# Performance work log

Measured on AMD Instinct MI355X. Metric: run time of the kernel, lower is better.

The kernel has to match this reference:

```python
import jax, jax.numpy as jnp
import numpy as np

B, S, D, H = 2, 2048, 1024, 16
HD = D // H  # head_dim = 64


def setup_inputs() -> dict:
    key = jax.random.key(0)
    k1, k2, k3 = jax.random.split(key, 3)
    x = jax.random.normal(k1, (B, S, D), dtype=jnp.float32)
    W_qkv = jax.random.normal(k2, (D, 3 * D), dtype=jnp.float32) * (D ** -0.5)
    b_qkv = jnp.zeros((3 * D,), dtype=jnp.float32)
    W_proj = jax.random.normal(k3, (D, D), dtype=jnp.float32) * (D ** -0.5)
    b_proj = jnp.zeros((D,), dtype=jnp.float32)
    return {"x": x, "W_qkv": W_qkv, "b_qkv": b_qkv, "W_proj": W_proj, "b_proj": b_proj}


def reference(x, W_qkv, b_qkv, W_proj, b_proj):
    b, s, d = x.shape
    scale = HD ** -0.5
    qkv = x @ W_qkv + b_qkv                       # [B,S,3D]
    q, k, v = jnp.split(qkv, 3, axis=-1)
    # [B,S,D] -> [B,H,S,HD]
    def to_heads(t):
        return t.reshape(b, s, H, HD).transpose(0, 2, 1, 3)
    q, k, v = map(to_heads, (q, k, v))
    scores = jnp.einsum('bhqd,bhkd->bhqk', q, k) * scale  # [B,H,S,S]
    causal = jnp.triu(jnp.ones((s, s), dtype=bool), k=1)
    scores = jnp.where(causal[None, None], -jnp.inf, scores)
    attn = jax.nn.softmax(scores, axis=-1)
    out = jnp.einsum('bhqk,bhkd->bhqd', attn, v)  # [B,H,S,HD]
    out = out.transpose(0, 2, 1, 3).reshape(b, s, d)
    return out @ W_proj + b_proj
```

## Files before the change

kernel.cpp:

```cpp
#include <hip/hip_runtime.h>

using frag_t = __attribute__((ext_vector_type(8))) short;
using f32x4  = __attribute__((ext_vector_type(4))) float;

#define L2E 1.4426950408889634f

#if __has_builtin(__builtin_amdgcn_exp2f)
#define EXP2(x) __builtin_amdgcn_exp2f(x)
#else
#define EXP2(x) exp2f(x)
#endif

constexpr int B_  = 2, S_ = 2048, D_ = 1024, H_ = 16, HD_ = 64;
constexpr float QSCALE = 0.125f * L2E;

__device__ __forceinline__ ushort f2bf(float f) {
  union { float f; unsigned u; } v; v.f = f;
  unsigned u = v.u;
  unsigned r = (u + 0x7FFFu + ((u >> 16) & 1u)) >> 16;
  return (ushort)r;
}

__device__ __forceinline__ void gld_lds16(const ushort* g, ushort* l) {
  __builtin_amdgcn_global_load_lds((const __attribute__((address_space(1))) void*)g,
                                   (__attribute__((address_space(3))) void*)l, 16, 0, 0);
}

__global__ __launch_bounds__(256) void k_prep(
    const float* __restrict__ x, const float* __restrict__ Wqkv,
    const float* __restrict__ Wproj,
    ushort* __restrict__ Xbf, ushort* __restrict__ Wqt, ushort* __restrict__ Wpt) {
  int blk = blockIdx.x, tid = threadIdx.x;
  if (blk < 1024) {
    size_t base = (size_t)blk * 4096 + tid * 4;
    #pragma unroll
    for (int i = 0; i < 4; ++i) {
      float4 f = *(const float4*)(x + base + i * 1024);
      ushort4 o;
      o.x = f2bf(f.x); o.y = f2bf(f.y); o.z = f2bf(f.z); o.w = f2bf(f.w);
      *(ushort4*)(Xbf + base + i * 1024) = o;
    }
  } else {
    __shared__ float tile[64][65];
    const float* in; ushort* out; int N, K, bx, by;
    if (blk < 1024 + 768) { int b2 = blk - 1024; in = Wqkv;  out = Wqt; N = 3072; K = 1024; bx = b2 % 48; by = b2 / 48; }
    else                  { int b2 = blk - 1792; in = Wproj; out = Wpt; N = 1024; K = 1024; bx = b2 % 16; by = b2 / 16; }
    int n0 = bx * 64, k0 = by * 64;
    int tx = tid & 63, ty = tid >> 6;
    #pragma unroll
    for (int i = 0; i < 16; ++i)
      tile[ty + i * 4][tx] = in[(size_t)(k0 + ty + i * 4) * N + n0 + tx];
    __syncthreads();
    #pragma unroll
    for (int i = 0; i < 16; ++i)
      out[(size_t)(n0 + ty + i * 4) * K + k0 + tx] = f2bf(tile[tx][ty + i * 4]);
  }
}

__global__ __launch_bounds__(512, 2) void k_gemm8(
    const ushort* __restrict__ A, const ushort* __restrict__ Bt,
    const float* __restrict__ bias,
    ushort* __restrict__ Qo, ushort* __restrict__ Ko, ushort* __restrict__ Vo) {
  __shared__ ushort smem[65536];
  int tid = threadIdx.x;
  int lane = tid & 63, wave = tid >> 6;
  int quad = lane >> 4, li = lane & 15;
  int wm = wave >> 1, wn = wave & 1;
  int wg = blockIdx.x;
  int bx = wg & 7, by = wg >> 3;
  int m0 = by * 128, n0 = bx * 384;
  const ushort* Asrc = A  + (size_t)m0 * 1024;
  const ushort* Bsrc = Bt + (size_t)n0 * 1024;
  int schunk = (tid & 3) ^ ((tid >> 4) & 3);
  int pos    = (quad ^ ((li >> 2) & 3)) * 8;

#define STGA(BI, KS, KT) \
    gld_lds16(&Asrc[(size_t)(tid >> 2) * 1024 + (KT)*64 + (KS)*32 + schunk*8], \
              &smem[(BI)*32768 + (KS)*4096 + wave*512])

#define STGB(BI, KS, KT) do { \
    _Pragma("unroll") \
    for (int p = 0; p < 3; ++p) \
      gld_lds16(&Bsrc[(size_t)(p*128 + (tid >> 2)) * 1024 + (KT)*64 + (KS)*32 + schunk*8], \
                &smem[(BI)*32768 + 8192 + (KS)*12288 + p*4096 + wave*512]); \
  } while (0)

  f32x4 acc[2][12] = {};
  frag_t af[2], bf[6];

#define PH(BI, KS, NH, STGS, W4) do { \
    if ((NH) == 0) { \
      _Pragma("unroll") \
      for (int mi = 0; mi < 2; ++mi) \
        af[mi] = *(const frag_t*)&smem[(BI)*32768 + (KS)*4096 + (wm*32 + mi*16 + li)*32 + pos]; \
    } \
    _Pragma("unroll") \
    for (int nj = 0; nj < 6; ++nj) \
      bf[nj] = *(const frag_t*)&smem[(BI)*32768 + 8192 + (KS)*12288 + (wn*192 + ((NH)*6 + nj)*16 + li)*32 + pos]; \
    STGS; \
    if (W4) asm volatile("s_waitcnt vmcnt(4)" ::: "memory"); \
    asm volatile("s_barrier" ::: "memory"); \
    __builtin_amdgcn_s_setprio(1); \
    _Pragma("unroll") \
    for (int mi = 0; mi < 2; ++mi) \
      _Pragma("unroll") \
      for (int nj = 0; nj < 6; ++nj) \
        acc[mi][(NH)*6 + nj] = __builtin_amdgcn_mfma_f32_16x16x32_bf16(af[mi], bf[nj], acc[mi][(NH)*6 + nj], 0, 0, 0); \
    __builtin_amdgcn_s_setprio(0); \
    asm volatile("s_barrier" ::: "memory"); \
  } while (0)

  STGA(0,0,0); STGB(0,0,0); STGA(0,1,0); STGB(0,1,0);
  STGA(1,0,1); STGB(1,0,1);
  asm volatile("s_waitcnt vmcnt(4)" ::: "memory");
  asm volatile("s_barrier" ::: "memory");

  for (int it = 0; it < 8; ++it) {
    int t1 = 2*it + 1;
    int t2 = (2*it + 2 < 16) ? 2*it + 2 : 15;
    int t3 = (2*it + 3 < 16) ? 2*it + 3 : 15;
    PH(0,0,0, STGA(1,1,t1), 0);
    PH(0,0,1, STGB(1,1,t1), 0);
    PH(0,1,0, STGA(0,0,t2), 0);
    PH(0,1,1, STGB(0,0,t2), 1);
    PH(1,0,0, STGA(0,1,t2), 0);
    PH(1,0,1, STGB(0,1,t2), 0);
    PH(1,1,0, STGA(1,0,t3), 0);
    PH(1,1,1, STGB(1,0,t3), 1);
  }
#undef PH
#undef STGA
#undef STGB

  asm volatile("s_waitcnt vmcnt(0)" ::: "memory");
  __syncthreads();

  #pragma unroll
  for (int nf = 0; nf < 12; ++nf) {
    int col0 = n0 + wn * 192 + nf * 16;
    int which = col0 >> 10;
    float bv = bias[col0 + li];
    if (which < 2) {
      int d = (col0 + li) & 1023;
      int h = d >> 6, hd = d & 63;
      #pragma unroll
      for (int mi = 0; mi < 2; ++mi)
        #pragma unroll
        for (int r = 0; r < 4; ++r) {
          int grow = m0 + wm * 32 + mi * 16 + quad * 4 + r;
          int b = grow >> 11, s = grow & 2047;
          size_t off = (((size_t)b * H_ + h) * S_ + s) * HD_ + hd;
          float v = acc[mi][nf][r] + bv;
          if (which == 0) Qo[off] = f2bf(v * QSCALE);
          else            Ko[off] = f2bf(v);
        }
    } else {
      ushort* vl = &smem[wave * 640];
      int gq = (quad == 1 || quad == 2) ? (quad ^ 3) : quad;
      #pragma unroll
      for (int mi = 0; mi < 2; ++mi) {
        union { ushort u[4]; uint2 w; } pk;
        #pragma unroll
        for (int r = 0; r < 4; ++r) pk.u[r] = f2bf(acc[mi][nf][r] + bv);
        *(uint2*)&vl[li * 40 + mi * 16 + gq * 4] = pk.w;
      }
      int h = (col0 >> 6) & 15, hd0 = col0 & 63;
      int b = m0 >> 11, s0 = (m0 & 2047) + wm * 32;
      int rt = lane >> 2, kc = (lane & 3) * 8;
      uint4 w = *(const uint4*)&vl[rt * 40 + kc];
      *(uint4*)&Vo[((size_t)(b * H_ + h) * HD_ + hd0 + rt) * S_ + s0 + kc] = w;
    }
  }
}

__global__ __launch_bounds__(256) void k_proj(
    const ushort* __restrict__ A, const ushort* __restrict__ Bt,
    const float* __restrict__ bias, float* __restrict__ Co) {
  constexpr int BM = 128, BN = 64, BK = 64, MI = 4, NI = 2;
  constexpr int N = 1024, K = 1024;
  __shared__ ushort smem[(BM + BN) * BK];
  ushort* As = smem;
  ushort* Bs = smem + BM * BK;
  int tid  = threadIdx.x;
  int lane = tid & 63, wave = tid >> 6;
  int quad = lane >> 4, li = lane & 15;
  int mbase = (wave >> 1) * (MI * 16);
  int nbase = (wave & 1) * 32;
  int m0 = blockIdx.y * BM, n0 = blockIdx.x * BN;
  int srow = lane >> 3;
  int scol = ((lane & 7) ^ srow) * 8;
  f32x4 acc[MI][NI] = {};
  for (int k0 = 0; k0 < K; k0 += BK) {
    #pragma unroll
    for (int i = 0; i < 4; ++i) {
      int rbase = i * 32 + wave * 8;
      gld_lds16(&A[(size_t)(m0 + rbase + srow) * K + k0 + scol], &As[rbase * BK]);
    }
    #pragma unroll
    for (int i = 0; i < 2; ++i) {
      int rbase = wave * 16 + i * 8;
      gld_lds16(&Bt[(size_t)(n0 + rbase + srow) * K + k0 + scol], &Bs[rbase * BK]);
    }
    __syncthreads();
    #pragma unroll
    for (int ks = 0; ks < 2; ++ks) {
      frag_t af[MI], bf[NI];
      #pragma unroll
      for (int mi = 0; mi < MI; ++mi)
        af[mi] = *(const frag_t*)&As[(mbase + mi * 16 + li) * BK + (((ks * 4 + quad) ^ (li & 7)) * 8)];
      #pragma unroll
      for (int ni = 0; ni < NI; ++ni)
        bf[ni] = *(const frag_t*)&Bs[(nbase + ni * 16 + li) * BK + (((ks * 4 + quad) ^ (li & 7)) * 8)];
      #pragma unroll
      for (int mi = 0; mi < MI; ++mi)
        #pragma unroll
        for (int ni = 0; ni < NI; ++ni)
          acc[mi][ni] = __builtin_amdgcn_mfma_f32_16x16x32_bf16(af[mi], bf[ni], acc[mi][ni], 0, 0, 0);
    }
    __syncthreads();
  }
  #pragma unroll
  for (int mi = 0; mi < MI; ++mi)
    #pragma unroll
    for (int ni = 0; ni < NI; ++ni) {
      int gcol = n0 + nbase + ni * 16 + li;
      float bv = bias[gcol];
      #pragma unroll
      for (int r = 0; r < 4; ++r) {
        int grow = m0 + mbase + mi * 16 + quad * 4 + r;
        Co[(size_t)grow * N + gcol] = acc[mi][ni][r] + bv;
      }
    }
}

__global__ __launch_bounds__(256) void k_attn(
    const ushort* __restrict__ Q, const ushort* __restrict__ K,
    const ushort* __restrict__ Vt, ushort* __restrict__ O) {
  __shared__ ushort Kbuf[2][64 * 64];
  __shared__ ushort Vbuf[2][64 * 64];
  int lane = threadIdx.x & 63, wave = threadIdx.x >> 6;
  int quad = lane >> 4, li = lane & 15;
  int bh = blockIdx.x;
  int yi = (int)blockIdx.y;
  int qb = (yi < 8) ? 31 - yi : (yi < 16) ? yi - 8 : (yi < 24) ? 39 - yi : yi - 16;
  int b = bh >> 4, hh = bh & 15;
  int q0 = qb * 64 + wave * 16;
  const ushort* Qb = Q  + (size_t)bh * S_ * HD_;
  const ushort* Kb = K  + (size_t)bh * S_ * HD_;
  const ushort* Vb = Vt + (size_t)bh * HD_ * S_;

  frag_t qf[2];
  #pragma unroll
  for (int ks = 0; ks < 2; ++ks)
    qf[ks] = *(const frag_t*)&Qb[(size_t)(q0 + li) * HD_ + ks * 32 + quad * 8];

  frag_t ones;
  #pragma unroll
  for (int i = 0; i < 8; ++i) ones[i] = (short)0x3F80;

  f32x4 o[4] = {};
  f32x4 lacc = {};

  auto stage = [&](int kb, int bi) {
    #pragma unroll
    for (int i = 0; i < 2; ++i) {
      int rt  = wave * 16 + i * 8 + (lane >> 3);
      int c16 = (lane & 7) ^ (lane >> 3);
      gld_lds16(&Kb[(size_t)(kb * 64 + rt) * HD_ + c16 * 8], &Kbuf[bi][(wave * 16 + i * 8) * 64]);
      gld_lds16(&Vb[(size_t)rt * S_ + kb * 64 + c16 * 8],    &Vbuf[bi][(wave * 16 + i * 8) * 64]);
    }
  };

  auto comp = [&](int kb, bool diag, int bi) {
    f32x4 sc[4];
    #pragma unroll
    for (int t = 0; t < 4; ++t) {
      f32x4 a = {};
      #pragma unroll
      for (int ks = 0; ks < 2; ++ks) {
        frag_t kf = *(const frag_t*)&Kbuf[bi][(t * 16 + li) * 64 + (((quad + ks * 4) ^ (li & 7)) * 8)];
        a = __builtin_amdgcn_mfma_f32_16x16x32_bf16(kf, qf[ks], a, 0, 0, 0);
      }
      sc[t] = a;
    }
    if (diag) {
      #pragma unroll
      for (int t = 0; t < 4; ++t) {
        int key = kb * 64 + t * 16 + quad * 4;
        #pragma unroll
        for (int r = 0; r < 4; ++r)
          if (key + r > q0 + li) sc[t][r] = -1e30f;
      }
    }
    #pragma unroll
    for (int t = 0; t < 4; ++t)
      #pragma unroll
      for (int r = 0; r < 4; ++r)
        sc[t][r] = EXP2(sc[t][r]);

    frag_t pf[2];
    #pragma unroll
    for (int ks = 0; ks < 2; ++ks) {
      unsigned w0e, w1e, w0o, w1o;
      asm("v_cvt_pk_bf16_f32 %0, %1, %2" : "=v"(w0e) : "v"(sc[2*ks][0]),   "v"(sc[2*ks][1]));
      asm("v_cvt_pk_bf16_f32 %0, %1, %2" : "=v"(w1e) : "v"(sc[2*ks][2]),   "v"(sc[2*ks][3]));
      asm("v_cvt_pk_bf16_f32 %0, %1, %2" : "=v"(w0o) : "v"(sc[2*ks+1][0]), "v"(sc[2*ks+1][1]));
      asm("v_cvt_pk_bf16_f32 %0, %1, %2" : "=v"(w1o) : "v"(sc[2*ks+1][2]), "v"(sc[2*ks+1][3]));
      asm("v_permlane32_swap_b32 %0, %1" : "+v"(w0e), "+v"(w0o));
      asm("v_permlane32_swap_b32 %0, %1" : "+v"(w1e), "+v"(w1o));
      union { frag_t f; unsigned u[4]; } pu;
      pu.u[0] = w0e; pu.u[1] = w1e; pu.u[2] = w0o; pu.u[3] = w1o;
      pf[ks] = pu.f;
    }
    lacc = __builtin_amdgcn_mfma_f32_16x16x32_bf16(ones, pf[0], lacc, 0, 0, 0);
    lacc = __builtin_amdgcn_mfma_f32_16x16x32_bf16(ones, pf[1], lacc, 0, 0, 0);
    #pragma unroll
    for (int ht = 0; ht < 4; ++ht)
      #pragma unroll
      for (int ks = 0; ks < 2; ++ks) {
        frag_t vtf = *(const frag_t*)&Vbuf[bi][(ht * 16 + li) * 64 + (((ks * 4 + quad) ^ (li & 7)) * 8)];
        o[ht] = __builtin_amdgcn_mfma_f32_16x16x32_bf16(vtf, pf[ks], o[ht], 0, 0, 0);
      }
  };

  stage(0, 0);
  __syncthreads();
  for (int kb = 0; kb <= qb; ++kb) {
    if (kb < qb) stage(kb + 1, (kb + 1) & 1);
    comp(kb, kb == qb, kb & 1);
    __syncthreads();
  }

  float inv = 1.f / lacc[0];
  int srow = q0 + li;
  size_t obase = ((size_t)b * S_ + srow) * D_ + hh * 64 + quad * 4;
  #pragma unroll
  for (int ht = 0; ht < 4; ++ht) {
    unsigned lo, hi;
    asm("v_cvt_pk_bf16_f32 %0, %1, %2" : "=v"(lo) : "v"(o[ht][0] * inv), "v"(o[ht][1] * inv));
    asm("v_cvt_pk_bf16_f32 %0, %1, %2" : "=v"(hi) : "v"(o[ht][2] * inv), "v"(o[ht][3] * inv));
    uint2 w; w.x = lo; w.y = hi;
    *(uint2*)&O[obase + ht * 16] = w;
  }
}

extern "C" void kernel_launch(void* const* d_in, const int* in_sizes, int n_in,
                              void* d_out, int out_size, void* d_ws, size_t ws_size,
                              hipStream_t stream) {
  (void)in_sizes; (void)n_in; (void)out_size; (void)ws_size;
  const float* x     = (const float*)d_in[0];
  const float* Wqkv  = (const float*)d_in[1];
  const float* bqkv  = (const float*)d_in[2];
  const float* Wproj = (const float*)d_in[3];
  const float* bproj = (const float*)d_in[4];
  float* out = (float*)d_out;

  char* ws = (char*)d_ws;
  ushort* Xbf = (ushort*)(ws);
  ushort* Wqt = (ushort*)(ws + (8u  << 20));
  ushort* Wpt = (ushort*)(ws + (14u << 20));
  ushort* Qbf = (ushort*)(ws + (16u << 20));
  ushort* Kbf = (ushort*)(ws + (24u << 20));
  ushort* Vtb = (ushort*)(ws + (32u << 20));
  ushort* Obf = Xbf;

  k_prep<<<dim3(2048), dim3(256), 0, stream>>>(x, Wqkv, Wproj, Xbf, Wqt, Wpt);
  k_gemm8<<<dim3(256), dim3(512), 0, stream>>>(Xbf, Wqt, bqkv, Qbf, Kbf, Vtb);
  k_attn<<<dim3(B_ * H_, 32), dim3(256), 0, stream>>>(Qbf, Kbf, Vtb, Obf);
  k_proj<<<dim3(16, 32), dim3(256), 0, stream>>>(Obf, Wpt, bproj, out);
}
```

Baseline: 167.4 us.

## Triple-buffer K/V staging with explicit vmcnt waits and skip masked diagonal tiles

The attention loop moves from double to triple-buffered LDS staging. It prefetches two key blocks ahead and replaces __syncthreads with a partial s_waitcnt vmcnt plus s_barrier, so one block's loads can stay in flight across the barrier. On the diagonal block, each wave also skips QK MFMAs, masking and exp for 16-key subtiles lying entirely above its causal boundary. The cost is 50% more LDS per block, which may reduce occupancy, and the hand-written vmcnt counts depend on the exact number of loads issued per stage.

```diff
diff --git a/kernel.cpp b/kernel.cpp
--- a/kernel.cpp
+++ b/kernel.cpp
@@ -236,8 +236,8 @@
 __global__ __launch_bounds__(256) void k_attn(
     const ushort* __restrict__ Q, const ushort* __restrict__ K,
     const ushort* __restrict__ Vt, ushort* __restrict__ O) {
-  __shared__ ushort Kbuf[2][64 * 64];
-  __shared__ ushort Vbuf[2][64 * 64];
+  __shared__ ushort Kbuf[3][64 * 64];
+  __shared__ ushort Vbuf[3][64 * 64];
   int lane = threadIdx.x & 63, wave = threadIdx.x >> 6;
   int quad = lane >> 4, li = lane & 15;
   int bh = blockIdx.x;
@@ -275,6 +275,7 @@
     f32x4 sc[4];
     #pragma unroll
     for (int t = 0; t < 4; ++t) {
+      if (diag && t > wave) { sc[t] = f32x4{0.f, 0.f, 0.f, 0.f}; continue; }
       f32x4 a = {};
       #pragma unroll
       for (int ks = 0; ks < 2; ++ks) {
@@ -286,6 +287,7 @@
     if (diag) {
       #pragma unroll
       for (int t = 0; t < 4; ++t) {
+        if (t > wave) continue;
         int key = kb * 64 + t * 16 + quad * 4;
         #pragma unroll
         for (int r = 0; r < 4; ++r)
@@ -293,10 +295,12 @@
       }
     }
     #pragma unroll
-    for (int t = 0; t < 4; ++t)
+    for (int t = 0; t < 4; ++t) {
+      if (diag && t > wave) continue;
       #pragma unroll
       for (int r = 0; r < 4; ++r)
         sc[t][r] = EXP2(sc[t][r]);
+    }
 
     frag_t pf[2];
     #pragma unroll
@@ -324,11 +328,28 @@
   };
 
   stage(0, 0);
-  __syncthreads();
+  if (qb >= 1) {
+    stage(1, 1);
+    asm volatile("s_waitcnt vmcnt(4)" ::: "memory");
+  } else {
+    asm volatile("s_waitcnt vmcnt(0)" ::: "memory");
+  }
+  asm volatile("s_barrier" ::: "memory");
+
+  int cur = 0;
   for (int kb = 0; kb <= qb; ++kb) {
-    if (kb < qb) stage(kb + 1, (kb + 1) & 1);
-    comp(kb, kb == qb, kb & 1);
-    __syncthreads();
+    bool more2 = (kb + 2 <= qb);
+    if (more2) {
+      int nxt2 = cur + 2; if (nxt2 >= 3) nxt2 -= 3;
+      stage(kb + 2, nxt2);
+    }
+    comp(kb, kb == qb, cur);
+    if (kb < qb) {
+      if (more2) asm volatile("s_waitcnt vmcnt(4)" ::: "memory");
+      else       asm volatile("s_waitcnt vmcnt(0)" ::: "memory");
+      asm volatile("s_barrier" ::: "memory");
+      cur = (cur == 2) ? 0 : cur + 1;
+    }
   }
 
   float inv = 1.f / lacc[0];
```

Result: no change. 168.1 us (+0.4%).
